# Kernel tuning notes

Measured on AMD Instinct MI355X. Metric: run time of the kernel, lower is better.

## Reference

```python
import jax, jax.numpy as jnp
import numpy as np

G, P_IN, P_OUT, C_Q = 4, 32, 128, 256
STRIDES = [4, 8, 16, 32]
TAU = 2.0
EPS = 1e-5


def _ln(x, axes):
    m = jnp.mean(x, axes, keepdims=True)
    v = jnp.var(x, axes, keepdims=True)
    return (x - m) * jax.lax.rsqrt(v + EPS)


def _grid_sample(value, pts):
    # torch F.grid_sample, bilinear, padding_mode='zeros', align_corners=False
    # value: [Bg, C, H, W], pts: [Bg, Q, P, 2] in [-1, 1] (x, y order)
    Bg, C, H, W = value.shape
    x = (pts[..., 0] + 1.0) * (W * 0.5) - 0.5
    y = (pts[..., 1] + 1.0) * (H * 0.5) - 0.5
    x0 = jnp.floor(x)
    y0 = jnp.floor(y)
    flat = value.reshape(Bg, C, H * W)
    Q, P = pts.shape[1], pts.shape[2]

    def corner(xf, yf, w):
        valid = (xf >= 0) & (xf <= W - 1) & (yf >= 0) & (yf <= H - 1)
        xi = jnp.clip(xf, 0, W - 1).astype(jnp.int32)
        yi = jnp.clip(yf, 0, H - 1).astype(jnp.int32)
        idx = (yi * W + xi).reshape(Bg, 1, Q * P)
        g = jnp.take_along_axis(flat, idx, axis=2).reshape(Bg, C, Q, P)
        return g * (w * valid)[:, None]

    out = (corner(x0, y0, (x0 + 1 - x) * (y0 + 1 - y))
           + corner(x0 + 1, y0, (x - x0) * (y0 + 1 - y))
           + corner(x0, y0 + 1, (x0 + 1 - x) * (y - y0))
           + corner(x0 + 1, y0 + 1, (x - x0) * (y - y0)))
    return out  # [Bg, C, Q, P]


def setup_inputs() -> dict:
    key = jax.random.key(0)
    ks = jax.random.split(key, 12)
    B, N = 2, 300
    sizes = [(200, 336), (100, 168), (50, 84), (25, 42)]
    xs = [jax.random.normal(ks[i], (B, 256, h, w), jnp.float32) for i, (h, w) in enumerate(sizes)]
    query_feat = jax.random.normal(ks[4], (B, N, C_Q), jnp.float32)
    u = jax.random.uniform(ks[5], (B, N, 4), jnp.float32)
    # xyzr roi: center x in [0,1344], y in [0,800], z (log2 scale) in [3,6], r in [-1,1]
    query_roi = jnp.stack([u[..., 0] * 1344.0, u[..., 1] * 800.0,
                           3.0 + 3.0 * u[..., 2], 2.0 * u[..., 3] - 1.0], axis=-1)
    w_off = jax.random.normal(ks[6], (C_Q, G * P_IN * 3), jnp.float32) * 0.01
    b = jax.random.uniform(ks[7], (G, P_IN, 3), jnp.float32, minval=-0.5, maxval=0.5)
    b_off = b.at[:, :, 2].set(-1.0).reshape(-1)
    cg = 256 // G
    total = G * (cg * cg + P_IN * P_OUT)
    pg_w = jax.random.normal(ks[8], (C_Q, total), jnp.float32) * 0.02
    pg_b = jax.random.normal(ks[9], (total,), jnp.float32) * 0.02
    op_w = jax.random.normal(ks[10], (G * P_OUT * cg, C_Q), jnp.float32) * 0.02
    op_b = jnp.zeros((C_Q,), jnp.float32)
    ln_g = jnp.ones((C_Q,), jnp.float32)
    ln_b = jnp.zeros((C_Q,), jnp.float32)
    return dict(x0=xs[0], x1=xs[1], x2=xs[2], x3=xs[3], query_feat=query_feat,
                query_roi=query_roi, w_off=w_off, b_off=b_off, pg_w=pg_w, pg_b=pg_b,
                op_w=op_w, op_b=op_b, ln_g=ln_g, ln_b=ln_b)


def reference(x0, x1, x2, x3, query_feat, query_roi, w_off, b_off,
              pg_w, pg_b, op_w, op_b, ln_g, ln_b):
    xs = [x0, x1, x2, x3]
    B, N, _ = query_feat.shape
    Cf = x0.shape[1]
    Cg = Cf // G
    L = len(xs)

    # ---- make_sample_points ----
    off = (query_feat @ w_off + b_off).reshape(B, N, G * P_IN, 3)
    xy = query_roi[..., :2]
    z = query_roi[..., 2:3]
    r = query_roi[..., 3:4]
    roi_wh = (2.0 ** z) * jnp.concatenate([2.0 ** (-0.5 * r), 2.0 ** (0.5 * r)], axis=-1)
    samp_xy = xy[:, :, None, :] + off[..., :2] * roi_wh[:, :, None, :]   # [B,N,GP,2]
    samp_lvl = z[:, :, None, :] + off[..., 2:3]                          # [B,N,GP,1]

    # ---- level weights: softmax(-(lvl-3 - l)^2 / tau) ----
    grid = jnp.arange(L, dtype=samp_lvl.dtype)
    lw = jax.nn.softmax(-(((samp_lvl - 3.0) - grid) ** 2) / TAU, axis=-1)  # [B,N,GP,L]

    # ---- multiscale sampling ----
    out = jnp.zeros((B * G, Cg, N, P_IN), x0.dtype)
    for i, (v, s) in enumerate(zip(xs, STRIDES)):
        H, W = v.shape[2], v.shape[3]
        size = jnp.array([W * s, H * s], samp_xy.dtype)
        pts = samp_xy / size * 2.0 - 1.0
        pts = pts.reshape(B, N, G, P_IN, 2).transpose(0, 2, 1, 3, 4).reshape(B * G, N, P_IN, 2)
        val = v.reshape(B * G, Cg, H, W)
        w = lw[..., i].reshape(B, N, G, P_IN).transpose(0, 2, 1, 3).reshape(B * G, 1, N, P_IN)
        out = out + _grid_sample(val, pts) * w
    sampled = out.reshape(B, G, Cg, N, P_IN).transpose(0, 3, 1, 4, 2)  # [B,N,G,P_IN,Cg]

    # ---- AdaptiveMixing ----
    params = (query_feat @ pg_w + pg_b).reshape(B, N, G, -1)
    M = params[..., :Cg * Cg].reshape(B, N, G, Cg, Cg)
    S = params[..., Cg * Cg:].reshape(B, N, G, P_OUT, P_IN)
    h = jnp.einsum('bngpc,bngcd->bngpd', sampled, M)
    h = jax.nn.relu(_ln(h, (-2, -1)))
    h = jnp.einsum('bngop,bngpc->bngoc', S, h)
    h = jax.nn.relu(_ln(h, (-2, -1)))
    q = query_feat + h.reshape(B, N, -1) @ op_w + op_b

    # ---- final LayerNorm (learned) ----
    return _ln(q, (-1,)) * ln_g + ln_b
```

## Files before the change

### kernel.cpp

```cpp
#include <hip/hip_runtime.h>
#include <cstdint>
#include <cstddef>

typedef __bf16 bf16;
typedef _Float16 f16;
typedef __attribute__((ext_vector_type(8))) __bf16 bf16x8;
typedef __attribute__((ext_vector_type(4))) __bf16 bf16x4;
typedef __attribute__((ext_vector_type(4))) float f32x4;

#define DINL __device__ __forceinline__

DINL float wred(float v) {
#pragma unroll
  for (int m = 32; m; m >>= 1) v += __shfl_xor(v, m, 64);
  return v;
}

DINL int swz(int r) { return ((r ^ (r >> 2)) & 7) << 4; }

__global__ void k_zero(float* __restrict__ p) {
  p[blockIdx.x * 256 + threadIdx.x] = 0.f;
}

__global__ void k_coords(const float* __restrict__ qf, const float* __restrict__ roi,
                         const float* __restrict__ w_off, const float* __restrict__ b_off,
                         float* __restrict__ coords) {
  int bn = blockIdx.x;
  int t = threadIdx.x;
  __shared__ float qs[256];
  __shared__ float offs[384];
  if (t < 256) qs[t] = qf[(size_t)bn * 256 + t];
  __syncthreads();
  float acc = b_off[t];
  for (int k = 0; k < 256; k++) acc += qs[k] * w_off[k * 384 + t];
  offs[t] = acc;
  __syncthreads();
  if (t < 128) {
    float ox = offs[t * 3 + 0], oy = offs[t * 3 + 1], oz = offs[t * 3 + 2];
    float cx = roi[bn * 4 + 0], cy = roi[bn * 4 + 1];
    float z  = roi[bn * 4 + 2], rr = roi[bn * 4 + 3];
    float sx = cx + ox * exp2f(z - 0.5f * rr);
    float sy = cy + oy * exp2f(z + 0.5f * rr);
    float lvl = z + oz;
    float e[4], mx = -1e30f;
#pragma unroll
    for (int l = 0; l < 4; l++) {
      float d = lvl - 3.0f - (float)l;
      e[l] = -d * d * 0.5f;
      mx = fmaxf(mx, e[l]);
    }
    float s = 0.f;
#pragma unroll
    for (int l = 0; l < 4; l++) { e[l] = expf(e[l] - mx); s += e[l]; }
    float inv = 1.f / s;
    float* o = coords + ((size_t)bn * 128 + t) * 6;
    o[0] = sx; o[1] = sy;
#pragma unroll
    for (int l = 0; l < 4; l++) o[2 + l] = e[l] * inv;
  }
}

__global__ __launch_bounds__(256) void k_xpose(
    const float* __restrict__ x0, const float* __restrict__ x1,
    const float* __restrict__ x2, const float* __restrict__ x3,
    f16* __restrict__ xt, int bg0, size_t slab) {
  const int HWl[4]  = {67200, 16800, 4200, 1050};
  const int RB[4]   = {0, 67200, 84000, 88200};
  const float* xs[4] = {x0, x1, x2, x3};
  int bg = bg0 + blockIdx.z;
  int b = bg >> 2, g = bg & 3;
  int l = blockIdx.y;
  int HW = HWl[l];
  int sp0 = blockIdx.x * 64;
  if (sp0 >= HW) return;
  const float* src = xs[l] + (size_t)(b * 256 + g * 64) * HW;
  __shared__ float tile[64][65];
  int tid = threadIdx.x;
  int lane = tid & 63, wv = tid >> 6;
#pragma unroll
  for (int j = 0; j < 16; j++) {
    int ch = j * 4 + wv;
    int sp = lane;
    if (sp0 + sp < HW) tile[sp][ch] = src[(size_t)ch * HW + sp0 + sp];
  }
  __syncthreads();
  f16* dst = xt + slab * blockIdx.z + (size_t)(RB[l] + sp0) * 64;
#pragma unroll
  for (int j = 0; j < 16; j++) {
    int sp = j * 4 + wv;
    int ch = lane;
    if (sp0 + sp < HW) dst[(size_t)sp * 64 + ch] = (f16)tile[sp][ch];
  }
}

__global__ __launch_bounds__(256) void k_sample2(
    const float* __restrict__ coords, const f16* __restrict__ xt,
    bf16* __restrict__ sampled, int bg0, size_t slab) {
  const int   Wl[4] = {336, 168, 84, 42};
  const int   Hl[4] = {200, 100, 50, 25};
  const int   RB[4] = {0, 67200, 84000, 88200};
  const float IS[4] = {0.25f, 0.125f, 0.0625f, 0.03125f};
  int bg = bg0 + blockIdx.z;
  int b = bg >> 2, g = bg & 3;
  int bn = b * 300 + blockIdx.x;
  const f16* xts = xt + slab * blockIdx.z;
  int c = threadIdx.x & 63, pp = threadIdx.x >> 6;
#pragma unroll
  for (int p8i = 0; p8i < 4; p8i++) {
    int p8 = blockIdx.y * 4 + p8i;
    int p = p8 * 4 + pp;
    const float* cd = coords + ((size_t)bn * 128 + g * 32 + p) * 6;
    float sx = cd[0], sy = cd[1];
    float acc = 0.f;
#pragma unroll
    for (int l = 0; l < 4; l++) {
      float wl = cd[2 + l];
      int W = Wl[l], H = Hl[l];
      float xf = sx * IS[l] - 0.5f;
      float yf = sy * IS[l] - 0.5f;
      float xx0 = floorf(xf), yy0 = floorf(yf);
      float fx = xf - xx0, fy = yf - yy0;
      int xi = (int)xx0, yi = (int)yy0;
      const f16* base = xts + (size_t)RB[l] * 64 + c;
      float v = 0.f;
      if (xi >= 0     && xi < W     && yi >= 0     && yi < H)
        v += (1.f - fx) * (1.f - fy) * (float)base[(size_t)(yi * W + xi) * 64];
      if (xi + 1 >= 0 && xi + 1 < W && yi >= 0     && yi < H)
        v += fx * (1.f - fy) * (float)base[(size_t)(yi * W + xi + 1) * 64];
      if (xi >= 0     && xi < W     && yi + 1 >= 0 && yi + 1 < H)
        v += (1.f - fx) * fy * (float)base[(size_t)((yi + 1) * W + xi) * 64];
      if (xi + 1 >= 0 && xi + 1 < W && yi + 1 >= 0 && yi + 1 < H)
        v += fx * fy * (float)base[(size_t)((yi + 1) * W + xi + 1) * 64];
      acc += wl * v;
    }
    sampled[(((size_t)bn * 4 + g) * 32 + p) * 64 + c] = (bf16)acc;
  }
}

__global__ __launch_bounds__(256) void k_params_mfma(
    const float* __restrict__ qf, const float* __restrict__ pg_w,
    const float* __restrict__ pg_b, bf16* __restrict__ pchunk,
    int m_off, int m_cnt) {
  __shared__ char sA[8192];
  __shared__ char sW[32768];
  const int tid = threadIdx.x;
  const int w = tid >> 6, l = tid & 63;
  const int lr = l & 15, lq = l >> 4;
  const int m0 = blockIdx.y * 64;
  const int n0 = blockIdx.x * 256;

  f32x4 acc[4][4];
#pragma unroll
  for (int i = 0; i < 4; i++)
#pragma unroll
    for (int j = 0; j < 4; j++) acc[i][j] = (f32x4)(0.f);

  for (int kt = 0; kt < 4; kt++) {
    const int kb = kt * 64;

#pragma unroll
    for (int i = 0; i < 2; i++) {
      int c = tid * 2 + i;
      int r = c >> 3, kc = c & 7;
      int gm = m0 + r; gm = (gm < m_cnt) ? gm : (m_cnt - 1);
      const float* src = qf + (size_t)(m_off + gm) * 256 + kb + kc * 8;
      f32x4 v0 = *(const f32x4*)src;
      f32x4 v1 = *(const f32x4*)(src + 4);
      bf16x8 t = {(bf16)v0[0], (bf16)v0[1], (bf16)v0[2], (bf16)v0[3],
                  (bf16)v1[0], (bf16)v1[1], (bf16)v1[2], (bf16)v1[3]};
      *(bf16x8*)(sA + r * 128 + ((kc << 4) ^ swz(r))) = t;
    }

#pragma unroll
    for (int i = 0; i < 4; i++) {
      int kblk = i * 4 + w;
      const float* src = pg_w + (size_t)(kb + kblk * 4) * 32768 + n0 + l * 4;
      f32x4 r0 = *(const f32x4*)(src);
      f32x4 r1 = *(const f32x4*)(src + 32768);
      f32x4 r2 = *(const f32x4*)(src + 65536);
      f32x4 r3 = *(const f32x4*)(src + 98304);
      int chv = (kblk >> 1) << 4;
      int sub = (kblk & 1) * 8;
#pragma unroll
      for (int j = 0; j < 4; j++) {
        int n = l * 4 + j;
        bf16x4 t = {(bf16)r0[j], (bf16)r1[j], (bf16)r2[j], (bf16)r3[j]};
        *(bf16x4*)(sW + n * 128 + (chv ^ swz(n)) + sub) = t;
      }
    }
    __syncthreads();

#pragma unroll
    for (int ks = 0; ks < 2; ks++) {
      bf16x8 a[4], b[4];
      int ch = (ks * 4 + lq) << 4;
#pragma unroll
      for (int i = 0; i < 4; i++) {
        int row = i * 16 + lr;
        a[i] = *(const bf16x8*)(sA + row * 128 + (ch ^ swz(row)));
      }
#pragma unroll
      for (int j = 0; j < 4; j++) {
        int nn = w * 64 + j * 16 + lr;
        b[j] = *(const bf16x8*)(sW + nn * 128 + (ch ^ swz(nn)));
      }
#pragma unroll
      for (int i = 0; i < 4; i++)
#pragma unroll
        for (int j = 0; j < 4; j++)
          acc[i][j] = __builtin_amdgcn_mfma_f32_16x16x32_bf16(a[i], b[j], acc[i][j], 0, 0, 0);
    }
    __syncthreads();
  }

#pragma unroll
  for (int i = 0; i < 4; i++) {
#pragma unroll
    for (int r = 0; r < 4; r++) {
      int m = m0 + i * 16 + lq * 4 + r;
      if (m < m_cnt) {
        bf16* dst = pchunk + (size_t)m * 32768 + n0 + w * 64 + lr;
#pragma unroll
        for (int j = 0; j < 4; j++) {
          int n = n0 + w * 64 + j * 16 + lr;
          dst[j * 16] = (bf16)(acc[i][j][r] + pg_b[n]);
        }
      }
    }
  }
}

__global__ __launch_bounds__(256) void k_mix_naive(
    const bf16* __restrict__ sampled, bf16* __restrict__ params, int m_off) {
  int bnl = blockIdx.x, g = blockIdx.y;
  int tid = threadIdx.x;
  __shared__ float samp_s[2048];
  __shared__ float h1[2048];
  __shared__ float h2[8192];
  __shared__ float red[8];
  const bf16* samp = sampled + ((size_t)(m_off + bnl) * 4 + g) * 2048;
  bf16* pr = params + (size_t)bnl * 32768 + (size_t)g * 8192;

#pragma unroll
  for (int j = 0; j < 8; j++) samp_s[tid + j * 256] = (float)samp[tid + j * 256];
  __syncthreads();

#pragma unroll
  for (int j = 0; j < 8; j++) {
    int e = tid + j * 256;
    int p = e >> 6, d = e & 63;
    float s = 0.f;
    for (int c = 0; c < 64; c++) s += samp_s[p * 64 + c] * (float)pr[c * 64 + d];
    h1[e] = s;
  }
  __syncthreads();

  {
    float s = 0.f, ss = 0.f;
#pragma unroll
    for (int j = 0; j < 8; j++) { float v = h1[tid + j * 256]; s += v; ss += v * v; }
    s = wred(s); ss = wred(ss);
    int w = tid >> 6;
    if ((tid & 63) == 0) { red[w] = s; red[4 + w] = ss; }
    __syncthreads();
    s = red[0] + red[1] + red[2] + red[3];
    ss = red[4] + red[5] + red[6] + red[7];
    float mean = s * (1.f / 2048.f);
    float var = ss * (1.f / 2048.f) - mean * mean;
    float rs = rsqrtf(fmaxf(var, 0.f) + 1e-5f);
    __syncthreads();
#pragma unroll
    for (int j = 0; j < 8; j++) {
      int e = tid + j * 256;
      float v = (h1[e] - mean) * rs;
      h1[e] = v > 0.f ? v : 0.f;
    }
  }
  __syncthreads();

#pragma unroll
  for (int j = 0; j < 32; j++) {
    int e = tid + j * 256;
    int o = e >> 6, d = e & 63;
    float s = 0.f;
    for (int p = 0; p < 32; p++) s += (float)pr[4096 + o * 32 + p] * h1[p * 64 + d];
    h2[e] = s;
  }
  __syncthreads();

  {
    float s = 0.f, ss = 0.f;
#pragma unroll
    for (int j = 0; j < 32; j++) { float v = h2[tid + j * 256]; s += v; ss += v * v; }
    s = wred(s); ss = wred(ss);
    int w = tid >> 6;
    if ((tid & 63) == 0) { red[w] = s; red[4 + w] = ss; }
    __syncthreads();
    s = red[0] + red[1] + red[2] + red[3];
    ss = red[4] + red[5] + red[6] + red[7];
    float mean = s * (1.f / 8192.f);
    float var = ss * (1.f / 8192.f) - mean * mean;
    float rs = rsqrtf(fmaxf(var, 0.f) + 1e-5f);
    __syncthreads();
#pragma unroll
    for (int j = 0; j < 32; j++) {
      int e = tid + j * 256;
      float v = (h2[e] - mean) * rs;
      v = v > 0.f ? v : 0.f;
      pr[e] = (bf16)v;
    }
  }
}

__global__ __launch_bounds__(256) void k_final_mfma(
    const bf16* __restrict__ pchunk, const float* __restrict__ op_w,
    float* __restrict__ facc, int m_off, int m_cnt, int KT) {
  __shared__ char sA[8192];
  __shared__ char sW[32768];
  const int tid = threadIdx.x;
  const int w = tid >> 6, l = tid & 63;
  const int lr = l & 15, lq = l >> 4;
  const int m0 = blockIdx.y * 64;
  const int kb0 = blockIdx.x * (KT * 64);

  f32x4 acc[4][4];
#pragma unroll
  for (int i = 0; i < 4; i++)
#pragma unroll
    for (int j = 0; j < 4; j++) acc[i][j] = (f32x4)(0.f);

  for (int kt = 0; kt < KT; kt++) {
    const int kb = kb0 + kt * 64;

#pragma unroll
    for (int i = 0; i < 2; i++) {
      int c = tid * 2 + i;
      int r = c >> 3, kc = c & 7;
      int gm = m0 + r; gm = (gm < m_cnt) ? gm : (m_cnt - 1);
      f32x4 v = *(const f32x4*)(pchunk + (size_t)gm * 32768 + kb + kc * 8);
      *(f32x4*)(sA + r * 128 + ((kc << 4) ^ swz(r))) = v;
    }

#pragma unroll
    for (int i = 0; i < 4; i++) {
      int kblk = i * 4 + w;
      const float* src = op_w + (size_t)(kb + kblk * 4) * 256 + l * 4;
      f32x4 r0 = *(const f32x4*)(src);
      f32x4 r1 = *(const f32x4*)(src + 256);
      f32x4 r2 = *(const f32x4*)(src + 512);
      f32x4 r3 = *(const f32x4*)(src + 768);
      int chv = (kblk >> 1) << 4;
      int sub = (kblk & 1) * 8;
#pragma unroll
      for (int j = 0; j < 4; j++) {
        int n = l * 4 + j;
        bf16x4 t = {(bf16)r0[j], (bf16)r1[j], (bf16)r2[j], (bf16)r3[j]};
        *(bf16x4*)(sW + n * 128 + (chv ^ swz(n)) + sub) = t;
      }
    }
    __syncthreads();

#pragma unroll
    for (int ks = 0; ks < 2; ks++) {
      bf16x8 a[4], b[4];
      int ch = (ks * 4 + lq) << 4;
#pragma unroll
      for (int i = 0; i < 4; i++) {
        int row = i * 16 + lr;
        a[i] = *(const bf16x8*)(sA + row * 128 + (ch ^ swz(row)));
      }
#pragma unroll
      for (int j = 0; j < 4; j++) {
        int n = w * 64 + j * 16 + lr;
        b[j] = *(const bf16x8*)(sW + n * 128 + (ch ^ swz(n)));
      }
#pragma unroll
      for (int i = 0; i < 4; i++)
#pragma unroll
        for (int j = 0; j < 4; j++)
          acc[i][j] = __builtin_amdgcn_mfma_f32_16x16x32_bf16(a[i], b[j], acc[i][j], 0, 0, 0);
    }
    __syncthreads();
  }

#pragma unroll
  for (int i = 0; i < 4; i++) {
#pragma unroll
    for (int r = 0; r < 4; r++) {
      int m = m0 + i * 16 + lq * 4 + r;
      if (m < m_cnt) {
        float* dst = facc + (size_t)(m_off + m) * 256 + w * 64 + lr;
#pragma unroll
        for (int j = 0; j < 4; j++)
          atomicAdd(dst + j * 16, acc[i][j][r]);
      }
    }
  }
}

__global__ void k_ln(const float* __restrict__ accbuf, const float* __restrict__ qf,
                     const float* __restrict__ opb, const float* __restrict__ lng,
                     const float* __restrict__ lnb, float* __restrict__ out) {
  int bn = blockIdx.x, t = threadIdx.x;
  float v = accbuf[bn * 256 + t] + qf[(size_t)bn * 256 + t] + opb[t];
  __shared__ float red[8];
  float s = wred(v), ss = wred(v * v);
  int w = t >> 6;
  if ((t & 63) == 0) { red[w] = s; red[4 + w] = ss; }
  __syncthreads();
  s = red[0] + red[1] + red[2] + red[3];
  ss = red[4] + red[5] + red[6] + red[7];
  float mean = s * (1.f / 256.f);
  float var = ss * (1.f / 256.f) - mean * mean;
  float y = (v - mean) * rsqrtf(fmaxf(var, 0.f) + 1e-5f);
  out[(size_t)bn * 256 + t] = y * lng[t] + lnb[t];
}

extern "C" void kernel_launch(void* const* d_in, const int* in_sizes, int n_in,
                              void* d_out, int out_size, void* d_ws, size_t ws_size,
                              hipStream_t stream) {
  const float* x0    = (const float*)d_in[0];
  const float* x1    = (const float*)d_in[1];
  const float* x2    = (const float*)d_in[2];
  const float* x3    = (const float*)d_in[3];
  const float* qf    = (const float*)d_in[4];
  const float* roi   = (const float*)d_in[5];
  const float* w_off = (const float*)d_in[6];
  const float* b_off = (const float*)d_in[7];
  const float* pg_w  = (const float*)d_in[8];
  const float* pg_b  = (const float*)d_in[9];
  const float* op_w  = (const float*)d_in[10];
  const float* op_b  = (const float*)d_in[11];
  const float* ln_g  = (const float*)d_in[12];
  const float* ln_b  = (const float*)d_in[13];
  float* out = (float*)d_out;

  const size_t SLAB = 5712000;
  const size_t NEEDED_BIG  = 143001600ull;
  const size_t NEEDED_SMALL = 31948800ull;
  if (ws_size < NEEDED_SMALL) return;

  char* ws = (char*)d_ws;
  float* coords  = (float*)(ws + 0);
  bf16*  sampled = (bf16*)(ws + 1843200);
  float* facc    = (float*)(ws + 11673600);

  k_zero<<<600, 256, 0, stream>>>(facc);
  k_coords<<<600, 384, 0, stream>>>(qf, roi, w_off, b_off, coords);

  if (ws_size >= NEEDED_BIG) {
    bf16* params = (bf16*)(ws + 12288000);
    f16*  xt     = (f16*)(ws + 51609600);
    k_xpose<<<dim3(1050, 4, 8), 256, 0, stream>>>(x0, x1, x2, x3, xt, 0, SLAB);
    k_sample2<<<dim3(300, 2, 8), 256, 0, stream>>>(coords, xt, sampled, 0, SLAB);
    k_params_mfma<<<dim3(128, 10), 256, 0, stream>>>(qf, pg_w, pg_b, params, 0, 600);
    k_mix_naive<<<dim3(600, 4), 256, 0, stream>>>(sampled, params, 0);
    k_final_mfma<<<dim3(64, 10), 256, 0, stream>>>(params, op_w, facc, 0, 600, 8);
  } else {
    bf16* pchunk = (bf16*)(ws + 12288000);
    f16*  xt     = (f16*)(ws + 12288000);
    for (int bg = 0; bg < 8; bg++) {
      k_xpose<<<dim3(1050, 4, 1), 256, 0, stream>>>(x0, x1, x2, x3, xt, bg, 0);
      k_sample2<<<dim3(300, 2, 1), 256, 0, stream>>>(coords, xt, sampled, bg, 0);
    }
    for (int chunk = 0; chunk < 2; chunk++) {
      int m_off = chunk * 300, m_cnt = 300;
      k_params_mfma<<<dim3(128, 5), 256, 0, stream>>>(qf, pg_w, pg_b, pchunk, m_off, m_cnt);
      k_mix_naive<<<dim3(300, 4), 256, 0, stream>>>(sampled, pchunk, m_off);
      k_final_mfma<<<dim3(32, 5), 256, 0, stream>>>(pchunk, op_w, facc, m_off, m_cnt, 16);
    }
  }

  k_ln<<<600, 256, 0, stream>>>(facc, qf, op_b, ln_g, ln_b, out);
}
```

Before: 612.1 us.

## Replace scalar adaptive-mixing kernel with MFMA bf16 matrix-core version

Rewrites the per-query/group adaptive mixing kernel so both small GEMMs (sampled x M and S x h1) run on bf16 MFMA 16x16x32 instructions instead of scalar FP32 loops over LDS. M is transposed into a swizzled LDS tile, the LayerNorm statistics are computed directly from the accumulator registers, and h1 is staged as bf16 in LDS. This removes heavy scalar FMA and LDS traffic, at the cost of bf16 rounding of the intermediate activations and more intricate indexing.

```diff
diff --git a/kernel.cpp b/kernel.cpp
--- a/kernel.cpp
+++ b/kernel.cpp
@@ -230,85 +230,120 @@
   }
 }
 
-__global__ __launch_bounds__(256) void k_mix_naive(
+__global__ __launch_bounds__(256) void k_mix_mfma(
     const bf16* __restrict__ sampled, bf16* __restrict__ params, int m_off) {
   int bnl = blockIdx.x, g = blockIdx.y;
   int tid = threadIdx.x;
-  __shared__ float samp_s[2048];
-  __shared__ float h1[2048];
-  __shared__ float h2[8192];
+  const int w = tid >> 6, l = tid & 63;
+  const int lr = l & 15, lq = l >> 4;
+  __shared__ char mt[8192];
+  __shared__ alignas(16) bf16 h1t[64 * 40];
   __shared__ float red[8];
   const bf16* samp = sampled + ((size_t)(m_off + bnl) * 4 + g) * 2048;
   bf16* pr = params + (size_t)bnl * 32768 + (size_t)g * 8192;
 
-#pragma unroll
-  for (int j = 0; j < 8; j++) samp_s[tid + j * 256] = (float)samp[tid + j * 256];
+  {
+    int cblk = tid >> 4, dblk = tid & 15;
+    const bf16* src = pr + cblk * 256 + dblk * 4;
+    bf16x4 r0 = *(const bf16x4*)(src);
+    bf16x4 r1 = *(const bf16x4*)(src + 64);
+    bf16x4 r2 = *(const bf16x4*)(src + 128);
+    bf16x4 r3 = *(const bf16x4*)(src + 192);
+    int chv = (cblk >> 1) << 4, sub = (cblk & 1) * 8;
+#pragma unroll
+    for (int j = 0; j < 4; j++) {
+      int d = dblk * 4 + j;
+      bf16x4 t = {r0[j], r1[j], r2[j], r3[j]};
+      *(bf16x4*)(mt + d * 128 + (chv ^ swz(d)) + sub) = t;
+    }
+  }
   __syncthreads();
 
-#pragma unroll
-  for (int j = 0; j < 8; j++) {
-    int e = tid + j * 256;
-    int p = e >> 6, d = e & 63;
-    float s = 0.f;
-    for (int c = 0; c < 64; c++) s += samp_s[p * 64 + c] * (float)pr[c * 64 + d];
-    h1[e] = s;
-  }
-  __syncthreads();
+  f32x4 acc1[2];
+  acc1[0] = (f32x4)(0.f); acc1[1] = (f32x4)(0.f);
+  const int dd = w * 16 + lr;
+#pragma unroll
+  for (int ks = 0; ks < 2; ks++) {
+    bf16x8 b = *(const bf16x8*)(mt + dd * 128 + ((((ks << 2) | lq) << 4) ^ swz(dd)));
+#pragma unroll
+    for (int i = 0; i < 2; i++) {
+      bf16x8 a = *(const bf16x8*)(samp + (i * 16 + lr) * 64 + ks * 32 + lq * 8);
+      acc1[i] = __builtin_amdgcn_mfma_f32_16x16x32_bf16(a, b, acc1[i], 0, 0, 0);
+    }
+  }
 
   {
     float s = 0.f, ss = 0.f;
 #pragma unroll
-    for (int j = 0; j < 8; j++) { float v = h1[tid + j * 256]; s += v; ss += v * v; }
+    for (int i = 0; i < 2; i++)
+#pragma unroll
+      for (int r = 0; r < 4; r++) { float v = acc1[i][r]; s += v; ss += v * v; }
     s = wred(s); ss = wred(ss);
-    int w = tid >> 6;
-    if ((tid & 63) == 0) { red[w] = s; red[4 + w] = ss; }
+    if (l == 0) { red[w] = s; red[4 + w] = ss; }
     __syncthreads();
     s = red[0] + red[1] + red[2] + red[3];
     ss = red[4] + red[5] + red[6] + red[7];
     float mean = s * (1.f / 2048.f);
     float var = ss * (1.f / 2048.f) - mean * mean;
     float rs = rsqrtf(fmaxf(var, 0.f) + 1e-5f);
-    __syncthreads();
-#pragma unroll
-    for (int j = 0; j < 8; j++) {
-      int e = tid + j * 256;
-      float v = (h1[e] - mean) * rs;
-      h1[e] = v > 0.f ? v : 0.f;
-    }
+#pragma unroll
+    for (int i = 0; i < 2; i++)
+#pragma unroll
+      for (int r = 0; r < 4; r++) {
+        float v = (acc1[i][r] - mean) * rs;
+        v = v > 0.f ? v : 0.f;
+        int p = i * 16 + lq * 4 + r;
+        h1t[dd * 40 + p] = (bf16)v;
+      }
   }
   __syncthreads();
 
-#pragma unroll
-  for (int j = 0; j < 32; j++) {
-    int e = tid + j * 256;
-    int o = e >> 6, d = e & 63;
-    float s = 0.f;
-    for (int p = 0; p < 32; p++) s += (float)pr[4096 + o * 32 + p] * h1[p * 64 + d];
-    h2[e] = s;
-  }
-  __syncthreads();
+  f32x4 acc2[2][4];
+#pragma unroll
+  for (int i = 0; i < 2; i++)
+#pragma unroll
+    for (int j = 0; j < 4; j++) acc2[i][j] = (f32x4)(0.f);
+  bf16x8 b2[4];
+#pragma unroll
+  for (int j = 0; j < 4; j++)
+    b2[j] = *(const bf16x8*)(&h1t[(j * 16 + lr) * 40 + lq * 8]);
+#pragma unroll
+  for (int i = 0; i < 2; i++) {
+    int o = w * 32 + i * 16 + lr;
+    bf16x8 a = *(const bf16x8*)(pr + 4096 + o * 32 + lq * 8);
+#pragma unroll
+    for (int j = 0; j < 4; j++)
+      acc2[i][j] = __builtin_amdgcn_mfma_f32_16x16x32_bf16(a, b2[j], acc2[i][j], 0, 0, 0);
+  }
 
   {
     float s = 0.f, ss = 0.f;
 #pragma unroll
-    for (int j = 0; j < 32; j++) { float v = h2[tid + j * 256]; s += v; ss += v * v; }
+    for (int i = 0; i < 2; i++)
+#pragma unroll
+      for (int j = 0; j < 4; j++)
+#pragma unroll
+        for (int r = 0; r < 4; r++) { float v = acc2[i][j][r]; s += v; ss += v * v; }
     s = wred(s); ss = wred(ss);
-    int w = tid >> 6;
-    if ((tid & 63) == 0) { red[w] = s; red[4 + w] = ss; }
+    if (l == 0) { red[w] = s; red[4 + w] = ss; }
     __syncthreads();
     s = red[0] + red[1] + red[2] + red[3];
     ss = red[4] + red[5] + red[6] + red[7];
     float mean = s * (1.f / 8192.f);
     float var = ss * (1.f / 8192.f) - mean * mean;
     float rs = rsqrtf(fmaxf(var, 0.f) + 1e-5f);
-    __syncthreads();
-#pragma unroll
-    for (int j = 0; j < 32; j++) {
-      int e = tid + j * 256;
-      float v = (h2[e] - mean) * rs;
-      v = v > 0.f ? v : 0.f;
-      pr[e] = (bf16)v;
-    }
+#pragma unroll
+    for (int i = 0; i < 2; i++)
+#pragma unroll
+      for (int r = 0; r < 4; r++) {
+        int o = w * 32 + i * 16 + lq * 4 + r;
+#pragma unroll
+        for (int j = 0; j < 4; j++) {
+          float v = (acc2[i][j][r] - mean) * rs;
+          v = v > 0.f ? v : 0.f;
+          pr[o * 64 + j * 16 + lr] = (bf16)v;
+        }
+      }
   }
 }
 
@@ -454,7 +489,7 @@
     k_xpose<<<dim3(1050, 4, 8), 256, 0, stream>>>(x0, x1, x2, x3, xt, 0, SLAB);
     k_sample2<<<dim3(300, 2, 8), 256, 0, stream>>>(coords, xt, sampled, 0, SLAB);
     k_params_mfma<<<dim3(128, 10), 256, 0, stream>>>(qf, pg_w, pg_b, params, 0, 600);
-    k_mix_naive<<<dim3(600, 4), 256, 0, stream>>>(sampled, params, 0);
+    k_mix_mfma<<<dim3(600, 4), 256, 0, stream>>>(sampled, params, 0);
     k_final_mfma<<<dim3(64, 10), 256, 0, stream>>>(params, op_w, facc, 0, 600, 8);
   } else {
     bf16* pchunk = (bf16*)(ws + 12288000);
@@ -466,7 +501,7 @@
     for (int chunk = 0; chunk < 2; chunk++) {
       int m_off = chunk * 300, m_cnt = 300;
       k_params_mfma<<<dim3(128, 5), 256, 0, stream>>>(qf, pg_w, pg_b, pchunk, m_off, m_cnt);
-      k_mix_naive<<<dim3(300, 4), 256, 0, stream>>>(sampled, pchunk, m_off);
+      k_mix_mfma<<<dim3(300, 4), 256, 0, stream>>>(sampled, pchunk, m_off);
       k_final_mfma<<<dim3(32, 5), 256, 0, stream>>>(pchunk, op_w, facc, m_off, m_cnt, 16);
     }
   }
```

Measured after the change: 513.7 us. 16.1% less time.
